# Kernel optimization log

Hardware: AMD Instinct MI355X
Metric: run time of the kernel (lower is better)

Reference implementation:

```python
import jax, jax.numpy as jnp
import numpy as np

B, N, C, P, H = 4096, 14, 512, 1024, 8  # batch, seq(=seg_sz), in_ch, proj_ch, heads
D = P // H                               # dim_head = 128
SCALE = D ** -0.5
EPS = 1e-5


def setup_inputs() -> dict:
    key = jax.random.key(0)
    ks = jax.random.split(key, 12)
    inp = {
        "x1": jax.random.normal(ks[0], (B, N, C), jnp.float32),
        "x2": jax.random.normal(ks[1], (B, N, C), jnp.float32),
        # hr: external per-batch gate over attention scores, broadcast over heads
        "hr": jax.random.uniform(ks[2], (B, N, N), jnp.float32),
        # Embedding(in_ch*2 -> proj_ch-256), modeled as Linear
        "W_emb": jax.random.normal(ks[3], (2 * C, P - 256), jnp.float32) * (2 * C) ** -0.5,
        "b_emb": jnp.zeros((P - 256,), jnp.float32),
        # learned absolute positional embedding [N, 256]
        "pos": jax.random.normal(ks[4], (N, 256), jnp.float32) * 0.02,
        # qkv projection, no bias (bias=False in source)
        "W_qkv": jax.random.normal(ks[5], (P, 3 * P), jnp.float32) * P ** -0.5,
        # post-attention LayerNorm
        "ln_g": jnp.ones((P,), jnp.float32),
        "ln_b": jnp.zeros((P,), jnp.float32),
        # FeedForward(P -> 1.5P -> P)
        "W1": jax.random.normal(ks[6], (P, int(P * 1.5)), jnp.float32) * P ** -0.5,
        "b1": jnp.zeros((int(P * 1.5),), jnp.float32),
        "W2": jax.random.normal(ks[7], (int(P * 1.5), P), jnp.float32) * (int(P * 1.5)) ** -0.5,
        "b2": jnp.zeros((P,), jnp.float32),
    }
    return inp


def _layernorm(x, g, b):
    mu = jnp.mean(x, axis=-1, keepdims=True)
    var = jnp.mean(jnp.square(x - mu), axis=-1, keepdims=True)
    return (x - mu) * jax.lax.rsqrt(var + EPS) * g + b


def reference(x1, x2, hr, W_emb, b_emb, pos, W_qkv, ln_g, ln_b, W1, b1, W2, b2):
    x = jnp.concatenate([x1, x2], axis=-1)                    # [B,N,2C]
    e = x @ W_emb + b_emb                                     # [B,N,P-256]
    pe = jnp.broadcast_to(pos, (x.shape[0],) + pos.shape)     # [B,N,256]
    x = jnp.concatenate([e, pe], axis=-1)                     # [B,N,P]
    res = x
    qkv = x @ W_qkv                                           # [B,N,3P]
    q, k, v = jnp.split(qkv, 3, axis=-1)
    def split_heads(t):
        return t.reshape(t.shape[0], t.shape[1], H, D).transpose(0, 2, 1, 3)  # [B,H,N,D]
    q, k, v = split_heads(q), split_heads(k), split_heads(v)
    dots = jnp.einsum('bhid,bhjd->bhij', q, k) * SCALE        # [B,H,N,N]
    attn = jax.nn.softmax(dots, axis=-1) * hr[:, None]        # post-softmax multiplicative gate
    # dropout = identity (eval mode)
    o = jnp.einsum('bhij,bhjd->bhid', attn, v)                # [B,H,N,D]
    o = o.transpose(0, 2, 1, 3).reshape(o.shape[0], N, P)     # [B,N,P]
    x = _layernorm(o + res, ln_g, ln_b)
    x = jax.nn.gelu(x @ W1 + b1) @ W2 + b2                    # FeedForward (dropout=identity)
    return x
```

## Files before the change

kernel.cpp:

```cpp
#include <hip/hip_runtime.h>
#include <hip/hip_bf16.h>
#include <cstdint>
#include <cstddef>

using bf16 = __hip_bfloat16;

typedef __attribute__((ext_vector_type(8))) short short8;
typedef __attribute__((ext_vector_type(4))) float fx4;

#define MROWS 57344

__device__ __forceinline__ float b2f(bf16 v) { return __bfloat162float(v); }
__device__ __forceinline__ bf16  f2b(float v) { return __float2bfloat16(v); }

union U2B { uint2 u; bf16 h[4]; };
union U4B { uint4 u; bf16 h[8]; };

#define GL2LDS(g, l)                                                  \
  __builtin_amdgcn_global_load_lds(                                   \
      (__attribute__((address_space(1))) void*)(g),                   \
      (__attribute__((address_space(3))) void*)(l), 16, 0, 0)

__global__ void detect_k(const uint32_t* __restrict__ g, int* __restrict__ flag) {
  if (threadIdx.x == 0) *flag = ((g[0] & 0xFFFFu) == 0x3F80u) ? 1 : 0;
}

__device__ __forceinline__ float loadAs(const void* p, size_t i, bool isbf) {
  return isbf ? b2f(((const bf16*)p)[i]) : ((const float*)p)[i];
}

__global__ void cvt8_k(const void* __restrict__ src, bf16* __restrict__ dst,
                       int n8, const int* __restrict__ flag) {
  const int i = blockIdx.x * 256 + threadIdx.x;
  if (i >= n8) return;
  U4B o;
  if (*flag) {
    o.u = ((const uint4*)src)[i];
  } else {
    const float* f = (const float*)src + (size_t)i * 8;
#pragma unroll
    for (int j = 0; j < 8; ++j) o.h[j] = f2b(f[j]);
  }
  ((uint4*)dst)[i] = o.u;
}

__global__ void transpose_k(const void* __restrict__ W, bf16* __restrict__ Wt,
                            int K, int N, const int* __restrict__ flag) {
  __shared__ float s[32][33];
  const bool isbf = (*flag != 0);
  const int n0 = blockIdx.x * 32, k0 = blockIdx.y * 32;
  const int tx = threadIdx.x, ty = threadIdx.y;
  for (int i = ty; i < 32; i += 8)
    s[i][tx] = loadAs(W, (size_t)(k0 + i) * N + n0 + tx, isbf);
  __syncthreads();
  for (int i = ty; i < 32; i += 8)
    Wt[(size_t)(n0 + i) * K + k0 + tx] = f2b(s[tx][i]);
}

__global__ void concat_k(const void* __restrict__ x1, const void* __restrict__ x2,
                         bf16* __restrict__ xcat, const int* __restrict__ flag) {
  const int m = blockIdx.x, j = threadIdx.x;
  const bool isbf = (*flag != 0);
  const void* src = (j < 64) ? x1 : x2;
  const int jj = (j < 64) ? j : j - 64;
  U4B o;
  if (isbf) {
    o.u = *(const uint4*)((const bf16*)src + (size_t)m * 512 + jj * 8);
  } else {
    const float* f = (const float*)src + (size_t)m * 512 + jj * 8;
#pragma unroll
    for (int q = 0; q < 8; ++q) o.h[q] = f2b(f[q]);
  }
  *(uint4*)(xcat + (size_t)m * 1024 + j * 8) = o.u;
}

__global__ void posfill_k(const void* __restrict__ pos, bf16* __restrict__ xp,
                          const int* __restrict__ flag) {
  const int m = blockIdx.x, j = threadIdx.x;
  xp[(size_t)m * 1024 + 768 + j] = f2b(loadAs(pos, (m % 14) * 256 + j, *flag != 0));
}

template <int EPI, int OUTDT>
__global__ __launch_bounds__(256, 2)
void gemm_bt(const bf16* __restrict__ A, const bf16* __restrict__ Bt,
             void* __restrict__ C, const bf16* __restrict__ bias,
             const int* __restrict__ dtflag, int M, int N, int K, int ldc) {
  __shared__ bf16 a_s[2 * 128 * 32];
  __shared__ bf16 b_s[2 * 128 * 32];

  const int t = threadIdx.x;
  const int w = t >> 6, L = t & 63, quad = L >> 4, l15 = L & 15;
  const int wr = w >> 1, wc = w & 1;

  const int gx = gridDim.x;
  const int nwg = gx * (int)gridDim.y;
  const int orig = (int)blockIdx.y * gx + (int)blockIdx.x;
  const int cpx = nwg >> 3;
  const int swz = (orig & 7) * cpx + (orig >> 3);
  const int m0 = (swz / gx) * 128, n0 = (swz % gx) * 128;

  const bool bfout = OUTDT ? (*dtflag != 0) : true;

  const int srow = L >> 2;
  const int scol = (L & 3) * 8;
  const bf16* gA = A + (size_t)(m0 + w * 32 + srow) * K + scol;
  const bf16* gB = Bt + (size_t)(n0 + w * 32 + srow) * K + scol;
  const size_t gstep = (size_t)16 * K;

  fx4 acc[4][4];
#pragma unroll
  for (int r = 0; r < 4; ++r)
#pragma unroll
    for (int c = 0; c < 4; ++c) acc[r][c] = fx4{0.f, 0.f, 0.f, 0.f};

  {
    bf16* lA = a_s + w * 1024;
    bf16* lB = b_s + w * 1024;
    GL2LDS(gA, lA);
    GL2LDS(gA + gstep, lA + 512);
    GL2LDS(gB, lB);
    GL2LDS(gB + gstep, lB + 512);
  }

  int cur = 0;
  for (int k0 = 0; k0 < K; k0 += 32) {
    const int nk = k0 + 32;
    if (nk < K) {
      bf16* lA = a_s + (cur ^ 1) * 4096 + w * 1024;
      bf16* lB = b_s + (cur ^ 1) * 4096 + w * 1024;
      GL2LDS(gA + nk, lA);
      GL2LDS(gA + gstep + nk, lA + 512);
      GL2LDS(gB + nk, lB);
      GL2LDS(gB + gstep + nk, lB + 512);
      asm volatile("s_waitcnt vmcnt(4)" ::: "memory");
    } else {
      asm volatile("s_waitcnt vmcnt(0)" ::: "memory");
    }
    __builtin_amdgcn_s_barrier();

    const bf16* as = a_s + cur * 4096;
    const bf16* bs = b_s + cur * 4096;
    short8 af[4], bfr[4];
#pragma unroll
    for (int r = 0; r < 4; ++r)
      af[r] = *(const short8*)(as + (wr * 64 + r * 16 + l15) * 32 + quad * 8);
#pragma unroll
    for (int c = 0; c < 4; ++c)
      bfr[c] = *(const short8*)(bs + (wc * 64 + c * 16 + l15) * 32 + quad * 8);
    asm volatile("s_waitcnt lgkmcnt(0)" ::: "memory");
    __builtin_amdgcn_sched_barrier(0);
#pragma unroll
    for (int r = 0; r < 4; ++r)
#pragma unroll
      for (int c = 0; c < 4; ++c)
        acc[r][c] = __builtin_amdgcn_mfma_f32_16x16x32_bf16(af[r], bfr[c],
                                                            acc[r][c], 0, 0, 0);
    asm volatile("" ::: "memory");
    __builtin_amdgcn_s_barrier();
    cur ^= 1;
  }

#pragma unroll
  for (int c = 0; c < 4; ++c) {
    const int col = n0 + wc * 64 + c * 16 + l15;
    float bv = 0.f;
    if (EPI >= 1) bv = b2f(bias[col]);
#pragma unroll
    for (int r = 0; r < 4; ++r) {
      const int rowb = m0 + wr * 64 + r * 16 + quad * 4;
#pragma unroll
      for (int g = 0; g < 4; ++g) {
        float x = acc[r][c][g] + bv;
        if (EPI == 2)
          x = x / (1.f + __expf(-1.5957691216f * (x + 0.044715f * x * x * x)));
        const size_t idx = (size_t)(rowb + g) * ldc + col;
        if (bfout) ((bf16*)C)[idx] = f2b(x);
        else       ((float*)C)[idx] = x;
      }
    }
  }
}

__global__ __launch_bounds__(256)
void attn_ln_k(const bf16* __restrict__ qkv, const bf16* __restrict__ xp,
               const bf16* __restrict__ hr, const bf16* __restrict__ ln_g,
               const bf16* __restrict__ ln_b, bf16* __restrict__ y) {
  constexpr int LD = 2056;
  __shared__ bf16 s_qk[14 * LD];
  __shared__ bf16 s_P[8 * 16 * 16];
  __shared__ float s_red[4][14][2];
  __shared__ float s_stats[14][2];

  const int b = blockIdx.x;
  const int t = threadIdx.x;
  const int w = t >> 6, L = t & 63, quad = L >> 4, l15 = L & 15;
  const size_t qkv_base = (size_t)b * 14 * 3072;

  for (int c = t; c < 3584; c += 256) {
    const int i = c >> 8, off = (c & 255) * 8;
    *(uint4*)(s_qk + i * LD + off) =
        *(const uint4*)(qkv + qkv_base + (size_t)i * 3072 + off);
  }
  __syncthreads();

  const int iq = (l15 < 14) ? l15 : 13;
#pragma unroll
  for (int hh = 0; hh < 2; ++hh) {
    const int h = w * 2 + hh;
    fx4 acc = fx4{0.f, 0.f, 0.f, 0.f};
#pragma unroll
    for (int kk = 0; kk < 4; ++kk) {
      short8 aq = *(const short8*)(s_qk + iq * LD + h * 128 + kk * 32 + quad * 8);
      short8 bk = *(const short8*)(s_qk + iq * LD + 1024 + h * 128 + kk * 32 + quad * 8);
      acc = __builtin_amdgcn_mfma_f32_16x16x32_bf16(aq, bk, acc, 0, 0, 0);
    }
    const int j = l15;
#pragma unroll
    for (int r = 0; r < 4; ++r) {
      float s = acc[r] * 0.08838834764831845f;
      if (j >= 14) s = -1e9f;
      float m = s;
#pragma unroll
      for (int mask = 1; mask < 16; mask <<= 1)
        m = fmaxf(m, __shfl_xor(m, mask, 16));
      const float e = __expf(s - m);
      float ssum = e;
#pragma unroll
      for (int mask = 1; mask < 16; mask <<= 1) ssum += __shfl_xor(ssum, mask, 16);
      float pr = e / ssum;
      const int i = quad * 4 + r;
      float gv = 0.f;
      if (i < 14 && j < 14)
        gv = pr * b2f(hr[(size_t)b * 196 + i * 14 + j]);
      s_P[h * 256 + i * 16 + j] = f2b(gv);
    }
  }
  __syncthreads();

  const int h = t >> 5, sub = t & 31;
  const int col = h * 128 + sub * 4;
  fx4 o[14];
#pragma unroll
  for (int i = 0; i < 14; ++i) o[i] = fx4{0.f, 0.f, 0.f, 0.f};
  for (int j = 0; j < 14; ++j) {
    U2B vv;
    vv.u = *(const uint2*)(qkv + qkv_base + (size_t)j * 3072 + 2048 + col);
    const float v0 = b2f(vv.h[0]), v1 = b2f(vv.h[1]),
                v2 = b2f(vv.h[2]), v3 = b2f(vv.h[3]);
#pragma unroll
    for (int i = 0; i < 14; ++i) {
      const float pij = b2f(s_P[h * 256 + i * 16 + j]);
      o[i][0] += pij * v0;
      o[i][1] += pij * v1;
      o[i][2] += pij * v2;
      o[i][3] += pij * v3;
    }
  }

  float sm[14], sq[14];
#pragma unroll
  for (int i = 0; i < 14; ++i) {
    U2B rr;
    rr.u = *(const uint2*)(xp + ((size_t)b * 14 + i) * 1024 + col);
    o[i][0] += b2f(rr.h[0]);
    o[i][1] += b2f(rr.h[1]);
    o[i][2] += b2f(rr.h[2]);
    o[i][3] += b2f(rr.h[3]);
    sm[i] = o[i][0] + o[i][1] + o[i][2] + o[i][3];
    sq[i] = o[i][0] * o[i][0] + o[i][1] * o[i][1] + o[i][2] * o[i][2] +
            o[i][3] * o[i][3];
  }
#pragma unroll
  for (int i = 0; i < 14; ++i) {
#pragma unroll
    for (int mask = 1; mask < 64; mask <<= 1) {
      sm[i] += __shfl_xor(sm[i], mask, 64);
      sq[i] += __shfl_xor(sq[i], mask, 64);
    }
  }
  if (L == 0) {
#pragma unroll
    for (int i = 0; i < 14; ++i) {
      s_red[w][i][0] = sm[i];
      s_red[w][i][1] = sq[i];
    }
  }
  __syncthreads();
  if (t < 14) {
    float S = 0.f, Q = 0.f;
#pragma unroll
    for (int ww = 0; ww < 4; ++ww) {
      S += s_red[ww][t][0];
      Q += s_red[ww][t][1];
    }
    const float mu = S * (1.f / 1024.f);
    const float var = Q * (1.f / 1024.f) - mu * mu;
    s_stats[t][0] = mu;
    s_stats[t][1] = rsqrtf(fmaxf(var, 0.f) + 1e-5f);
  }
  __syncthreads();

  U2B gg, bb;
  gg.u = *(const uint2*)(ln_g + col);
  bb.u = *(const uint2*)(ln_b + col);
#pragma unroll
  for (int i = 0; i < 14; ++i) {
    const float mu = s_stats[i][0], rs = s_stats[i][1];
    U2B ov;
    ov.h[0] = f2b((o[i][0] - mu) * rs * b2f(gg.h[0]) + b2f(bb.h[0]));
    ov.h[1] = f2b((o[i][1] - mu) * rs * b2f(gg.h[1]) + b2f(bb.h[1]));
    ov.h[2] = f2b((o[i][2] - mu) * rs * b2f(gg.h[2]) + b2f(bb.h[2]));
    ov.h[3] = f2b((o[i][3] - mu) * rs * b2f(gg.h[3]) + b2f(bb.h[3]));
    *(uint2*)(y + ((size_t)b * 14 + i) * 1024 + col) = ov.u;
  }
}

extern "C" void kernel_launch(void* const* d_in, const int* in_sizes, int n_in,
                              void* d_out, int out_size, void* d_ws,
                              size_t ws_size, hipStream_t stream) {
  const void* x1    = d_in[0];
  const void* x2    = d_in[1];
  const void* hr    = d_in[2];
  const void* W_emb = d_in[3];
  const void* b_emb = d_in[4];
  const void* pos   = d_in[5];
  const void* W_qkv = d_in[6];
  const void* ln_g  = d_in[7];
  const void* ln_b  = d_in[8];
  const void* W1    = d_in[9];
  const void* b1    = d_in[10];
  const void* W2    = d_in[11];
  const void* b2    = d_in[12];

  bf16* ws = (bf16*)d_ws;
  int* flag = (int*)d_ws;
  size_t off = 8;
  auto alloc = [&](size_t n) { bf16* p = ws + off; off += n; return p; };
  bf16* WembT = alloc((size_t)768 * 1024);
  bf16* WqkvT = alloc((size_t)3072 * 1024);
  bf16* W1T   = alloc((size_t)1536 * 1024);
  bf16* W2T   = alloc((size_t)1024 * 1536);
  bf16* bembB = alloc(768);
  bf16* b1B   = alloc(1536);
  bf16* b2B   = alloc(1024);
  bf16* lngB  = alloc(1024);
  bf16* lnbB  = alloc(1024);
  bf16* hrB   = alloc((size_t)4096 * 196);
  bf16* xp    = alloc((size_t)MROWS * 1024);
  bf16* qkv   = alloc((size_t)MROWS * 3072);
  bf16* xcat  = qkv;
  bf16* mid   = qkv;
  bf16* yb    = (bf16*)d_out;

  detect_k<<<1, 64, 0, stream>>>((const uint32_t*)ln_g, flag);

  const dim3 tb(32, 8);
  transpose_k<<<dim3(768 / 32, 1024 / 32), tb, 0, stream>>>(W_emb, WembT, 1024, 768, flag);
  transpose_k<<<dim3(3072 / 32, 1024 / 32), tb, 0, stream>>>(W_qkv, WqkvT, 1024, 3072, flag);
  transpose_k<<<dim3(1536 / 32, 1024 / 32), tb, 0, stream>>>(W1, W1T, 1024, 1536, flag);
  transpose_k<<<dim3(1024 / 32, 1536 / 32), tb, 0, stream>>>(W2, W2T, 1536, 1024, flag);

  cvt8_k<<<1, 256, 0, stream>>>(b_emb, bembB, 96, flag);
  cvt8_k<<<1, 256, 0, stream>>>(b1, b1B, 192, flag);
  cvt8_k<<<1, 256, 0, stream>>>(b2, b2B, 128, flag);
  cvt8_k<<<1, 256, 0, stream>>>(ln_g, lngB, 128, flag);
  cvt8_k<<<1, 256, 0, stream>>>(ln_b, lnbB, 128, flag);
  cvt8_k<<<392, 256, 0, stream>>>(hr, hrB, 100352, flag);

  concat_k<<<MROWS, 128, 0, stream>>>(x1, x2, xcat, flag);
  posfill_k<<<MROWS, 256, 0, stream>>>(pos, xp, flag);

  gemm_bt<1, 0><<<dim3(6, MROWS / 128), 256, 0, stream>>>(
      xcat, WembT, xp, bembB, nullptr, MROWS, 768, 1024, 1024);
  gemm_bt<0, 0><<<dim3(24, MROWS / 128), 256, 0, stream>>>(
      xp, WqkvT, qkv, nullptr, nullptr, MROWS, 3072, 1024, 3072);
  attn_ln_k<<<4096, 256, 0, stream>>>(qkv, xp, hrB, lngB, lnbB, yb);
  gemm_bt<2, 0><<<dim3(12, MROWS / 128), 256, 0, stream>>>(
      yb, W1T, mid, b1B, nullptr, MROWS, 1536, 1024, 1536);
  gemm_bt<1, 1><<<dim3(8, MROWS / 128), 256, 0, stream>>>(
      mid, W2T, d_out, b2B, flag, MROWS, 1024, 1536, 1024);
}
```

Measured before the change: 2.063 ms.

## Stage GEMM epilogue through LDS for vectorized stores; drop block swizzle

The GEMM epilogue now writes each 16-row slab of accumulators into a per-wave LDS scratch area that reuses the operand buffers. It then reads the slab back transposed so each lane emits a 4-wide vector store (uint2 for bf16, float4 for fp32) instead of scattered scalar stores. This is meant to cut the number of global store transactions and improve coalescing on the large output writes. The change also removes the grouped workgroup-index swizzle in favour of plain row-major tile mapping, which may reduce L2 reuse of the A and B tiles. It adds LDS round trips and waits in the epilogue.

```diff
diff --git a/kernel.cpp b/kernel.cpp
--- a/kernel.cpp
+++ b/kernel.cpp
@@ -85,20 +85,14 @@
 void gemm_bt(const bf16* __restrict__ A, const bf16* __restrict__ Bt,
              void* __restrict__ C, const bf16* __restrict__ bias,
              const int* __restrict__ dtflag, int M, int N, int K, int ldc) {
-  __shared__ bf16 a_s[2 * 128 * 32];
-  __shared__ bf16 b_s[2 * 128 * 32];
+  __shared__ bf16 smem[16384];
+  bf16* a_s = smem;
+  bf16* b_s = smem + 8192;
 
   const int t = threadIdx.x;
   const int w = t >> 6, L = t & 63, quad = L >> 4, l15 = L & 15;
   const int wr = w >> 1, wc = w & 1;
-
-  const int gx = gridDim.x;
-  const int nwg = gx * (int)gridDim.y;
-  const int orig = (int)blockIdx.y * gx + (int)blockIdx.x;
-  const int cpx = nwg >> 3;
-  const int swz = (orig & 7) * cpx + (orig >> 3);
-  const int m0 = (swz / gx) * 128, n0 = (swz % gx) * 128;
-
+  const int m0 = blockIdx.y * 128, n0 = blockIdx.x * 128;
   const bool bfout = OUTDT ? (*dtflag != 0) : true;
 
   const int srow = L >> 2;
@@ -160,24 +154,46 @@
     cur ^= 1;
   }
 
-#pragma unroll
-  for (int c = 0; c < 4; ++c) {
-    const int col = n0 + wc * 64 + c * 16 + l15;
-    float bv = 0.f;
-    if (EPI >= 1) bv = b2f(bias[col]);
-#pragma unroll
-    for (int r = 0; r < 4; ++r) {
-      const int rowb = m0 + wr * 64 + r * 16 + quad * 4;
+  float* eps = (float*)smem + (size_t)w * 1088;
+  const int erow = L >> 2;
+  const int ec0  = L & 3;
+
+  float bv[4] = {0.f, 0.f, 0.f, 0.f};
+  if (EPI >= 1) {
+#pragma unroll
+    for (int c = 0; c < 4; ++c) bv[c] = b2f(bias[n0 + wc * 64 + c * 16 + l15]);
+  }
+
+#pragma unroll
+  for (int r = 0; r < 4; ++r) {
+#pragma unroll
+    for (int c = 0; c < 4; ++c) {
 #pragma unroll
       for (int g = 0; g < 4; ++g) {
-        float x = acc[r][c][g] + bv;
+        float x = acc[r][c][g] + bv[c];
         if (EPI == 2)
           x = x / (1.f + __expf(-1.5957691216f * (x + 0.044715f * x * x * x)));
-        const size_t idx = (size_t)(rowb + g) * ldc + col;
-        if (bfout) ((bf16*)C)[idx] = f2b(x);
-        else       ((float*)C)[idx] = x;
+        eps[(quad * 4 + g) * 68 + c * 16 + l15] = x;
       }
     }
+    asm volatile("s_waitcnt lgkmcnt(0)" ::: "memory");
+    __builtin_amdgcn_sched_barrier(0);
+    const int grow = m0 + wr * 64 + r * 16 + erow;
+#pragma unroll
+    for (int i = 0; i < 4; ++i) {
+      const int cc = ec0 * 4 + i * 16;
+      fx4 v = *(const fx4*)(eps + erow * 68 + cc);
+      const size_t cbase = (size_t)grow * ldc + n0 + wc * 64 + cc;
+      if (bfout) {
+        U2B pk;
+        pk.h[0] = f2b(v[0]); pk.h[1] = f2b(v[1]);
+        pk.h[2] = f2b(v[2]); pk.h[3] = f2b(v[3]);
+        *(uint2*)((bf16*)C + cbase) = pk.u;
+      } else {
+        *(fx4*)((float*)C + cbase) = v;
+      }
+    }
+    __builtin_amdgcn_sched_barrier(0);
   }
 }
 
```

Result: no change. 2.067 ms (+0.2%).
